# Kernel optimization log

Measured on AMD Instinct MI355X. Metric: run time of the kernel, lower is better.

## Reference

```python
import jax, jax.numpy as jnp
import numpy as np

N, D, E, K, CAP = 16384, 1024, 64, 2, 640

def setup_inputs() -> dict:
    key = jax.random.key(0)
    k1, k2, k3 = jax.random.split(key, 3)
    x = jax.random.normal(k1, (N, D), dtype=jnp.float32)
    Wr = jax.random.normal(k2, (D, E), dtype=jnp.float32) / np.sqrt(D)
    br = jnp.zeros((E,), dtype=jnp.float32)
    We = jax.random.normal(k3, (E, D, D), dtype=jnp.float32) / np.sqrt(D)
    return {"x": x, "Wr": Wr, "br": br, "We": We, "k": K, "capacity": CAP}

def _route(x, Wr, br, k, num_experts):
    logits = x @ Wr + br                                  # [N, E]
    top_k_vals, top_k_idxs = jax.lax.top_k(logits, k)     # [N, k]
    gates = jax.nn.softmax(top_k_vals, axis=-1)           # [N, k]
    # flatten k-major like the original: transpose((1,0)).flatten()
    flat = top_k_idxs.T.reshape(-1)                       # [k*N]
    expert_mask = (flat[:, None] == jnp.arange(num_experts)).astype(jnp.int32)
    buffer_idxs = jnp.cumsum(expert_mask, axis=0) * expert_mask - 1  # [k*N, E]
    buffer_idxs = buffer_idxs.reshape(k, -1, num_experts)            # [k, N, E]
    dispatch_idxs = buffer_idxs.transpose(2, 0, 1).max(axis=1)       # [E, N]
    combine_idxs = buffer_idxs.max(axis=-1).T                        # [N, k]
    return gates, top_k_idxs, dispatch_idxs, combine_idxs

def reference(x, Wr, br, We, k, capacity):
    num_experts = Wr.shape[1]
    gates, top_k_idxs, dispatch_idxs, combine_idxs = _route(x, Wr, br, k, num_experts)
    # dispatch: scatter tokens into per-expert capacity buffers; unassigned (-1)
    # and overflow (>= capacity) tokens land in the dropped slot `capacity`.
    d_idx = jnp.where((dispatch_idxs < 0) | (dispatch_idxs > capacity), capacity, dispatch_idxs)
    def scatter_one(idx):
        return jnp.zeros((capacity + 1, x.shape[-1]), x.dtype).at[idx].set(x)[:-1]
    dispatched = jax.vmap(scatter_one)(d_idx)             # [E, C, D]
    # per-expert linear (the wrap()/vmap-ed expert), grouped GEMM
    expert_out = jax.nn.relu(jnp.einsum('ecd,edh->ech', dispatched, We))
    # combine: gather back, pad row `capacity` yields zeros for dropped tokens
    padded = jnp.pad(expert_out, ((0, 0), (0, 1), (0, 0)))
    c_idx = jnp.where((combine_idxs < 0) | (combine_idxs > capacity), capacity, combine_idxs)
    combined = padded[top_k_idxs, c_idx]                  # [N, k, D]
    return jnp.einsum('nk,nkd->nd', gates, combined)      # [N, D]
```

## Files before the change

### kernel.cpp

```cpp
#include <hip/hip_runtime.h>
#include <hip/hip_bf16.h>
#include <cstdint>
#include <cstddef>

#define N_TOK 16384
#define DIM   1024
#define NEXP  64
#define CAPACITY 640

typedef __bf16 bf16x8 __attribute__((ext_vector_type(8)));
typedef float  f32x4  __attribute__((ext_vector_type(4)));

__device__ __forceinline__ unsigned short f2bf(float f) {
    union { float f; unsigned int u; } a; a.f = f;
    unsigned int r = a.u + 0x7FFFu + ((a.u >> 16) & 1u);
    return (unsigned short)(r >> 16);
}

__global__ __launch_bounds__(256) void router_kernel(
    const float* __restrict__ x, const float* __restrict__ Wr,
    const float* __restrict__ br, unsigned short* __restrict__ xb,
    int* __restrict__ top2i, float* __restrict__ gates2)
{
    __shared__ float xs[64][68];
    __shared__ float wT[64][68];
    const int tid = threadIdx.x;
    const int t0  = blockIdx.x * 64;
    const int tm  = tid >> 4;
    const int te  = tid & 15;

    float acc[4][4];
#pragma unroll
    for (int i = 0; i < 4; i++)
#pragma unroll
        for (int j = 0; j < 4; j++) acc[i][j] = 0.f;

    for (int ks = 0; ks < DIM; ks += 64) {
        __syncthreads();
#pragma unroll
        for (int l = 0; l < 4; l++) {
            int row = l * 16 + tm;
            int col = te * 4;
            float4 v = *(const float4*)(x + (size_t)(t0 + row) * DIM + ks + col);
            *(float4*)&xs[row][col] = v;
            ushort4 b = make_ushort4(f2bf(v.x), f2bf(v.y), f2bf(v.z), f2bf(v.w));
            *(ushort4*)(xb + (size_t)(t0 + row) * DIM + ks + col) = b;
        }
#pragma unroll
        for (int l = 0; l < 4; l++) {
            int kr = l * 16 + tm;
            int ec = te * 4;
            float4 v = *(const float4*)(Wr + (size_t)(ks + kr) * NEXP + ec);
            wT[ec + 0][kr] = v.x; wT[ec + 1][kr] = v.y;
            wT[ec + 2][kr] = v.z; wT[ec + 3][kr] = v.w;
        }
        __syncthreads();
#pragma unroll 4
        for (int kk = 0; kk < 64; kk += 4) {
            float4 xv[4], wv[4];
#pragma unroll
            for (int i = 0; i < 4; i++) xv[i] = *(float4*)&xs[tm + i * 16][kk];
#pragma unroll
            for (int j = 0; j < 4; j++) wv[j] = *(float4*)&wT[te + j * 16][kk];
#pragma unroll
            for (int i = 0; i < 4; i++)
#pragma unroll
                for (int j = 0; j < 4; j++)
                    acc[i][j] += xv[i].x * wv[j].x + xv[i].y * wv[j].y +
                                 xv[i].z * wv[j].z + xv[i].w * wv[j].w;
        }
    }
    __syncthreads();
#pragma unroll
    for (int i = 0; i < 4; i++)
#pragma unroll
        for (int j = 0; j < 4; j++)
            xs[tm + i * 16][te + j * 16] = acc[i][j] + br[te + j * 16];
    __syncthreads();
    if (tid < 64) {
        int n = t0 + tid;
        float v1 = -1e30f, v2 = -1e30f; int i1 = 0, i2 = 0;
        for (int e = 0; e < 64; e++) {
            float v = xs[tid][e];
            if (v > v1)      { v2 = v1; i2 = i1; v1 = v; i1 = e; }
            else if (v > v2) { v2 = v;  i2 = e; }
        }
        float g0 = 1.f / (1.f + expf(v2 - v1));
        top2i[n * 2 + 0] = i1; top2i[n * 2 + 1] = i2;
        gates2[n * 2 + 0] = g0; gates2[n * 2 + 1] = 1.f - g0;
    }
}

__global__ __launch_bounds__(256) void hist_kernel(
    const int* __restrict__ top2i, int* __restrict__ hist)
{
    __shared__ int cnt[NEXP];
    int tid = threadIdx.x;
    if (tid < NEXP) cnt[tid] = 0;
    __syncthreads();
    int p = blockIdx.x * 256 + tid;
    int k = p >> 14, n = p & 16383;
    int e = top2i[n * 2 + k];
    atomicAdd(&cnt[e], 1);
    __syncthreads();
    if (tid < NEXP) hist[blockIdx.x * NEXP + tid] = cnt[tid];
}

__global__ __launch_bounds__(64) void scan_kernel(
    const int* __restrict__ hist, int* __restrict__ pre, int* __restrict__ cntc)
{
    int e = threadIdx.x;
    int run = 0;
#pragma unroll 8
    for (int c = 0; c < 128; c++) {
        pre[c * NEXP + e] = run;
        run += hist[c * NEXP + e];
    }
    cntc[e] = run < CAPACITY ? run : CAPACITY;
}

__global__ __launch_bounds__(64) void rank_kernel(
    const int* __restrict__ top2i, const float* __restrict__ gates2,
    const int* __restrict__ pre, int* __restrict__ list_tok,
    float* __restrict__ list_gate)
{
    int lane = threadIdx.x;
    int c = blockIdx.x;
    int cnt_reg = pre[c * NEXP + lane];
    unsigned long long below = (1ull << lane) - 1ull;
    for (int r = 0; r < 4; r++) {
        int p = c * 256 + r * 64 + lane;
        int k = p >> 14, n = p & 16383;
        int e = top2i[n * 2 + k];
        int slot = 0;
#pragma unroll 1
        for (int q = 0; q < NEXP; q++) {
            unsigned long long mask = __ballot(e == q);
            int base = __shfl(cnt_reg, q);
            if (e == q) slot = base + __popcll(mask & below);
            if (lane == q) cnt_reg += (int)__popcll(mask);
        }
        if (slot < CAPACITY) {
            list_tok[e * CAPACITY + slot]  = n;
            list_gate[e * CAPACITY + slot] = gates2[n * 2 + k];
        }
    }
}

#define MT 128
#define NT 128
#define BK 32
#define LDA 36

__global__ __launch_bounds__(256) void moe_gemm(
    const unsigned short* __restrict__ xb, const float* __restrict__ We,
    const int* __restrict__ list_tok, const float* __restrict__ list_gate,
    const int* __restrict__ cntc, float* __restrict__ out)
{
    const int bid = blockIdx.x;
    const int e   = bid / 40;
    const int rem = bid % 40;
    const int mt  = rem >> 3;
    const int nt  = rem & 7;
    const int cnt = cntc[e];
    if (mt * MT >= cnt) return;
    int valid = cnt - mt * MT; if (valid > MT) valid = MT;

    __shared__ unsigned short As[MT * LDA];
    __shared__ unsigned short Bs[NT * LDA];
    __shared__ int   tok_s[MT];
    __shared__ float gate_s[MT];

    const int tid = threadIdx.x;
    if (tid < MT) {
        int slot = mt * MT + tid;
        bool v = tid < valid;
        tok_s[tid]  = v ? list_tok[e * CAPACITY + slot]  : list_tok[e * CAPACITY];
        gate_s[tid] = v ? list_gate[e * CAPACITY + slot] : 0.f;
    }
    __syncthreads();

    const int arow = tid >> 1, ah = tid & 1;
    const unsigned short* aptr = xb + (size_t)tok_s[arow] * DIM + ah * 16;
    const int bn0 = (tid & 31) * 4;
    const int bkr = (tid >> 5) * 4;
    const float* bptr = We + (size_t)e * DIM * DIM + (size_t)bkr * DIM + nt * NT + bn0;

    f32x4 acc[4][4];
#pragma unroll
    for (int i = 0; i < 4; i++)
#pragma unroll
        for (int j = 0; j < 4; j++) acc[i][j] = (f32x4){0.f, 0.f, 0.f, 0.f};

    const int lane = tid & 63, wave = tid >> 6;
    const int wm = wave >> 1, wn = wave & 1;
    const int fm = lane & 15, kq = lane >> 4;

    for (int ks = 0; ks < DIM; ks += BK) {
        __syncthreads();
        uint4 a0 = *(const uint4*)(aptr + ks);
        uint4 a1 = *(const uint4*)(aptr + ks + 8);
        {
            unsigned short* d = &As[arow * LDA + ah * 16];
            *(uint2*)(d + 0)  = make_uint2(a0.x, a0.y);
            *(uint2*)(d + 4)  = make_uint2(a0.z, a0.w);
            *(uint2*)(d + 8)  = make_uint2(a1.x, a1.y);
            *(uint2*)(d + 12) = make_uint2(a1.z, a1.w);
        }
        {
            float4 b[4];
#pragma unroll
            for (int j = 0; j < 4; j++)
                b[j] = *(const float4*)(bptr + (size_t)(ks + j) * DIM);
            union { float4 v; float f[4]; } u0, u1, u2, u3;
            u0.v = b[0]; u1.v = b[1]; u2.v = b[2]; u3.v = b[3];
#pragma unroll
            for (int cc = 0; cc < 4; cc++) {
                unsigned int lo = (unsigned int)f2bf(u0.f[cc]) | ((unsigned int)f2bf(u1.f[cc]) << 16);
                unsigned int hi = (unsigned int)f2bf(u2.f[cc]) | ((unsigned int)f2bf(u3.f[cc]) << 16);
                *(uint2*)&Bs[(bn0 + cc) * LDA + bkr] = make_uint2(lo, hi);
            }
        }
        __syncthreads();
        union { uint2 u[2]; bf16x8 v; } fa[4], fb[4];
#pragma unroll
        for (int i = 0; i < 4; i++) {
            const unsigned short* s = &As[(wm * 64 + i * 16 + fm) * LDA + kq * 8];
            fa[i].u[0] = *(const uint2*)(s);
            fa[i].u[1] = *(const uint2*)(s + 4);
        }
#pragma unroll
        for (int j = 0; j < 4; j++) {
            const unsigned short* s = &Bs[(wn * 64 + j * 16 + fm) * LDA + kq * 8];
            fb[j].u[0] = *(const uint2*)(s);
            fb[j].u[1] = *(const uint2*)(s + 4);
        }
#pragma unroll
        for (int i = 0; i < 4; i++)
#pragma unroll
            for (int j = 0; j < 4; j++)
                acc[i][j] = __builtin_amdgcn_mfma_f32_16x16x32_bf16(
                    fa[i].v, fb[j].v, acc[i][j], 0, 0, 0);
    }

    const int col0 = nt * NT + wn * 64 + fm;
#pragma unroll
    for (int i = 0; i < 4; i++) {
        int rbase = wm * 64 + i * 16 + kq * 4;
#pragma unroll
        for (int j = 0; j < 4; j++) {
            int col = col0 + j * 16;
#pragma unroll
            for (int r = 0; r < 4; r++) {
                int row = rbase + r;
                if (row < valid) {
                    float v = acc[i][j][r];
                    v = fmaxf(v, 0.f) * gate_s[row];
                    atomicAdd(out + (size_t)tok_s[row] * DIM + col, v);
                }
            }
        }
    }
}

extern "C" void kernel_launch(void* const* d_in, const int* in_sizes, int n_in,
                              void* d_out, int out_size, void* d_ws, size_t ws_size,
                              hipStream_t stream)
{
    const float* x  = (const float*)d_in[0];
    const float* Wr = (const float*)d_in[1];
    const float* br = (const float*)d_in[2];
    const float* We = (const float*)d_in[3];
    float* out = (float*)d_out;

    char* ws = (char*)d_ws;
    size_t off = 0;
    unsigned short* xb = (unsigned short*)(ws + off); off += (size_t)N_TOK * DIM * 2;
    int*   top2i     = (int*)(ws + off);   off += (size_t)N_TOK * 2 * 4;
    float* gates2    = (float*)(ws + off); off += (size_t)N_TOK * 2 * 4;
    int*   hist      = (int*)(ws + off);   off += 128 * NEXP * 4;
    int*   pre       = (int*)(ws + off);   off += 128 * NEXP * 4;
    int*   cntc      = (int*)(ws + off);   off += NEXP * 4;
    int*   list_tok  = (int*)(ws + off);   off += NEXP * CAPACITY * 4;
    float* list_gate = (float*)(ws + off); off += NEXP * CAPACITY * 4;

    hipMemsetAsync(out, 0, (size_t)N_TOK * DIM * 4, stream);
    router_kernel<<<N_TOK / 64, 256, 0, stream>>>(x, Wr, br, xb, top2i, gates2);
    hist_kernel<<<128, 256, 0, stream>>>(top2i, hist);
    scan_kernel<<<1, 64, 0, stream>>>(hist, pre, cntc);
    rank_kernel<<<128, 64, 0, stream>>>(top2i, gates2, pre, list_tok, list_gate);
    moe_gemm<<<NEXP * 40, 256, 0, stream>>>(xb, We, list_tok, list_gate, cntc, out);
}
```

Baseline: 675.0 us.

## Pre-convert expert weights to packed bf16 and use direct-to-LDS loads in GEMM

Adds a kernel that converts the fp32 expert weights to bf16 once per call, stored in a K-packed tiled layout, and a new grouped GEMM that streams A and B tiles into LDS with global_load_lds and MFMA 16x16x32 bf16. This halves the weight bytes the GEMM reads and removes per-tile conversion work inside it. In exchange it adds a full conversion pass over 256 MB of fp32 weights and needs a larger workspace, falling back to the old kernel when the workspace is too small. The GEMM loop has no double buffering.

```diff
diff --git a/kernel.cpp b/kernel.cpp
--- a/kernel.cpp
+++ b/kernel.cpp
@@ -147,6 +147,134 @@
     }
 }
 
+__global__ __launch_bounds__(256) void convert_we(
+    const float* __restrict__ We, unsigned short* __restrict__ WeB)
+{
+    const int b   = blockIdx.x;
+    const int e   = b >> 7;
+    const int nt  = (b >> 4) & 7;
+    const int ksi = b & 15;
+    __shared__ __align__(16) unsigned short T[64][132];
+    const int tid = threadIdx.x;
+    const int tc  = (tid & 31) * 4;
+    const int tr  = tid >> 5;
+    const float* src = We + ((size_t)e << 20) + (size_t)(ksi * 64) * DIM + nt * 128;
+#pragma unroll
+    for (int l = 0; l < 8; l++) {
+        int dr = l * 8 + tr;
+        float4 v = *(const float4*)(src + (size_t)dr * DIM + tc);
+        ushort4 u = make_ushort4(f2bf(v.x), f2bf(v.y), f2bf(v.z), f2bf(v.w));
+        *(ushort4*)&T[dr][tc] = u;
+    }
+    __syncthreads();
+    unsigned short* dst = WeB + ((size_t)b << 13);
+#pragma unroll
+    for (int i = 0; i < 4; i++) {
+        int p = i * 256 + tid;
+        int kq = p >> 7, col = p & 127;
+        unsigned int w0 = (unsigned int)T[kq * 8 + 0][col] | ((unsigned int)T[kq * 8 + 1][col] << 16);
+        unsigned int w1 = (unsigned int)T[kq * 8 + 2][col] | ((unsigned int)T[kq * 8 + 3][col] << 16);
+        unsigned int w2 = (unsigned int)T[kq * 8 + 4][col] | ((unsigned int)T[kq * 8 + 5][col] << 16);
+        unsigned int w3 = (unsigned int)T[kq * 8 + 6][col] | ((unsigned int)T[kq * 8 + 7][col] << 16);
+        *(uint4*)(dst + (size_t)p * 8) = make_uint4(w0, w1, w2, w3);
+    }
+}
+
+__global__ __launch_bounds__(256) void moe_gemm2(
+    const unsigned short* __restrict__ xb, const unsigned short* __restrict__ WeB,
+    const int* __restrict__ list_tok, const float* __restrict__ list_gate,
+    const int* __restrict__ cntc, float* __restrict__ out)
+{
+    const int bid = blockIdx.x;
+    const int e   = bid / 40;
+    const int rem = bid % 40;
+    const int mt  = rem >> 3;
+    const int nt  = rem & 7;
+    const int cnt = cntc[e];
+    if (mt * 128 >= cnt) return;
+    int valid = cnt - mt * 128; if (valid > 128) valid = 128;
+
+    __shared__ __align__(16) unsigned short As[8 * 128 * 8];
+    __shared__ __align__(16) unsigned short Bs[8 * 128 * 8];
+    __shared__ int   tok_s[128];
+    __shared__ float gate_s[128];
+
+    const int tid = threadIdx.x;
+    if (tid < 128) {
+        int slot = mt * 128 + tid;
+        bool v = tid < valid;
+        tok_s[tid]  = v ? list_tok[e * CAPACITY + slot]  : list_tok[e * CAPACITY];
+        gate_s[tid] = v ? list_gate[e * CAPACITY + slot] : 0.f;
+    }
+    __syncthreads();
+
+    const int arow  = tid & 127;
+    const int ahalf = tid >> 7;
+    const unsigned short* aG = xb + (size_t)tok_s[arow] * DIM + ahalf * 8;
+    const unsigned short* bG = WeB + ((size_t)(e * 8 + nt) * 16) * 8192 + (size_t)tid * 8;
+
+    const int wv   = tid >> 6;
+    const int lane = tid & 63;
+    const int wm = wv >> 1, wn = wv & 1;
+    const int fm = lane & 15, kq = lane >> 4;
+
+    f32x4 acc[4][4];
+#pragma unroll
+    for (int i = 0; i < 4; i++)
+#pragma unroll
+        for (int j = 0; j < 4; j++) acc[i][j] = (f32x4){0.f, 0.f, 0.f, 0.f};
+
+    for (int ksi = 0; ksi < 16; ksi++) {
+        __syncthreads();
+#pragma unroll
+        for (int i = 0; i < 4; i++) {
+            const int ldsOff = (i * 256 + wv * 64) * 8;
+            __builtin_amdgcn_global_load_lds(
+                (const __attribute__((address_space(1))) unsigned int*)(aG + ksi * 64 + i * 16),
+                (__attribute__((address_space(3))) unsigned int*)(As + ldsOff), 16, 0, 0);
+            __builtin_amdgcn_global_load_lds(
+                (const __attribute__((address_space(1))) unsigned int*)(bG + (size_t)ksi * 8192 + i * 2048),
+                (__attribute__((address_space(3))) unsigned int*)(Bs + ldsOff), 16, 0, 0);
+        }
+        __syncthreads();
+#pragma unroll
+        for (int kk = 0; kk < 2; kk++) {
+            union { uint4 u; bf16x8 v; } fa[4], fb[4];
+#pragma unroll
+            for (int i = 0; i < 4; i++)
+                fa[i].u = *(const uint4*)(As + ((kk * 4 + kq) * 128 + wm * 64 + i * 16 + fm) * 8);
+#pragma unroll
+            for (int j = 0; j < 4; j++)
+                fb[j].u = *(const uint4*)(Bs + ((kk * 4 + kq) * 128 + wn * 64 + j * 16 + fm) * 8);
+#pragma unroll
+            for (int i = 0; i < 4; i++)
+#pragma unroll
+                for (int j = 0; j < 4; j++)
+                    acc[i][j] = __builtin_amdgcn_mfma_f32_16x16x32_bf16(
+                        fa[i].v, fb[j].v, acc[i][j], 0, 0, 0);
+        }
+    }
+
+    const int col0 = nt * 128 + wn * 64 + fm;
+#pragma unroll
+    for (int i = 0; i < 4; i++) {
+        int rbase = wm * 64 + i * 16 + kq * 4;
+#pragma unroll
+        for (int j = 0; j < 4; j++) {
+            int col = col0 + j * 16;
+#pragma unroll
+            for (int r = 0; r < 4; r++) {
+                int row = rbase + r;
+                if (row < valid) {
+                    float v = acc[i][j][r];
+                    v = fmaxf(v, 0.f) * gate_s[row];
+                    atomicAdd(out + (size_t)tok_s[row] * DIM + col, v);
+                }
+            }
+        }
+    }
+}
+
 #define MT 128
 #define NT 128
 #define BK 32
@@ -283,11 +411,21 @@
     int*   cntc      = (int*)(ws + off);   off += NEXP * 4;
     int*   list_tok  = (int*)(ws + off);   off += NEXP * CAPACITY * 4;
     float* list_gate = (float*)(ws + off); off += NEXP * CAPACITY * 4;
+    off = (off + 255) & ~(size_t)255;
+    unsigned short* WeB = (unsigned short*)(ws + off);
+    size_t need = off + (size_t)NEXP * DIM * DIM * 2;
+
+    const bool fast = ws_size >= need;
 
     hipMemsetAsync(out, 0, (size_t)N_TOK * DIM * 4, stream);
+    if (fast)
+        convert_we<<<NEXP * 8 * 16, 256, 0, stream>>>(We, WeB);
     router_kernel<<<N_TOK / 64, 256, 0, stream>>>(x, Wr, br, xb, top2i, gates2);
     hist_kernel<<<128, 256, 0, stream>>>(top2i, hist);
     scan_kernel<<<1, 64, 0, stream>>>(hist, pre, cntc);
     rank_kernel<<<128, 64, 0, stream>>>(top2i, gates2, pre, list_tok, list_gate);
-    moe_gemm<<<NEXP * 40, 256, 0, stream>>>(xb, We, list_tok, list_gate, cntc, out);
-}
+    if (fast)
+        moe_gemm2<<<NEXP * 40, 256, 0, stream>>>(xb, WeB, list_tok, list_gate, cntc, out);
+    else
+        moe_gemm<<<NEXP * 40, 256, 0, stream>>>(xb, We, list_tok, list_gate, cntc, out);
+}
```

Result: slower. 743.6 us (+10.2%).
